# Kernel tuning notes

Measured on AMD Instinct MI355X. Metric: run time of the kernel, lower is better.

Reference implementation:

```python
import jax, jax.numpy as jnp
import numpy as np

B, S, E, D, H = 4, 2048, 512, 64, 8
NEG = float(np.finfo(np.float64).min)  # tf uses tf.float64.min; overflows to -inf in fp32, same softmax effect


def setup_inputs() -> dict:
    key = jax.random.key(0)
    ks = jax.random.split(key, 6)
    std = 0.05  # tf.random_normal_initializer default stddev
    x = jax.random.normal(ks[0], (B, S, E), dtype=jnp.float32)
    Wq = jax.random.normal(ks[1], (H, E, D), dtype=jnp.float32) * std
    Wk = jax.random.normal(ks[2], (H, E, D), dtype=jnp.float32) * std
    Wvd = jax.random.normal(ks[3], (H, E, D), dtype=jnp.float32) * std
    Wvu = jax.random.normal(ks[4], (H, D, E), dtype=jnp.float32) * std
    Wo = jax.random.normal(ks[5], (H, 1), dtype=jnp.float32) * std
    return {"x": x, "Wq": Wq, "Wk": Wk, "Wvd": Wvd, "Wvu": Wvu, "Wo": Wo}


def reference(x, Wq, Wk, Wvd, Wvu, Wo):
    # Per-head projections, vectorized over the head axis h
    Q = jnp.einsum("bse,hed->bhsd", x, Wq)  # [B,H,S,D]
    K = jnp.einsum("bse,hed->bhsd", x, Wk)
    score = jnp.einsum("bhsd,bhtd->bhst", Q, K) / jnp.sqrt(jnp.float32(D))
    # tf.linalg.band_part(score, -1, 0): keep lower triangle (causal)
    tril = jnp.tril(jnp.ones((S, S), dtype=bool))
    score = jnp.where(tril, score, 0.0)
    # tf.where(score != 0, score, float64.min): masks zeros (incl. any exact-zero kept entries)
    score = jnp.where(score != 0, score, jnp.float32(NEG))
    attn = jax.nn.softmax(score, axis=-1)  # [B,H,S,S]
    # low-rank value projection: x @ (Wvdown @ Wvup) per head
    Wv = jnp.einsum("hed,hdf->hef", Wvd, Wvu)  # [H,E,E]
    V = jnp.einsum("bse,hef->bhsf", x, Wv)      # [B,H,S,E]
    heads = jnp.einsum("bhst,bhte->bhse", attn, V)  # [B,H,S,E]
    # stack on last axis then matmul with Wo[H,1] == weighted sum over heads
    out = jnp.einsum("bhse,h->bse", heads, Wo[:, 0])
    return out
```

## Files before the change

kernel.cpp:

```cpp
#include <hip/hip_runtime.h>
#include <math.h>
#include <type_traits>

namespace {
constexpr int B = 4, S = 2048, E = 512, D = 64, H = 8;
constexpr int KD = 512;

typedef short bf8 __attribute__((ext_vector_type(8)));
typedef short bf4 __attribute__((ext_vector_type(4)));
typedef float f4 __attribute__((ext_vector_type(4)));

__device__ __forceinline__ short f2bf(float f) {
  union { float f; unsigned u; } v; v.f = f;
  const unsigned r = v.u + 0x7fffu + ((v.u >> 16) & 1u);
  return (short)(r >> 16);
}

__device__ __forceinline__ unsigned cvt_pk_bf16(float a, float b) {
  unsigned r;
  asm("v_cvt_pk_bf16_f32 %0, %1, %2" : "=v"(r) : "v"(a), "v"(b));
  return r;
}

__device__ __forceinline__ void gload16(const void* g, void* l) {
  __builtin_amdgcn_global_load_lds(
      (const __attribute__((address_space(1))) unsigned int*)g,
      (__attribute__((address_space(3))) unsigned int*)l, 16, 0, 0);
}

__global__ __launch_bounds__(256) void prep_kernel(
    const float* __restrict__ x, const float* __restrict__ Wq,
    const float* __restrict__ Wk, const float* __restrict__ Wvd,
    const float* __restrict__ Wvu, const float* __restrict__ Wo,
    short* __restrict__ xb, short* __restrict__ WcatT,
    short* __restrict__ W2T) {
  __shared__ float T[64][65];
  const int bid = blockIdx.x;
  const int tid = threadIdx.x;
  if (bid < 2048) {
    const size_t i = ((size_t)bid * 256 + tid) * 8;
    const float4 v0 = *(const float4*)(x + i);
    const float4 v1 = *(const float4*)(x + i + 4);
    bf8 o;
    o[0] = f2bf(v0.x); o[1] = f2bf(v0.y); o[2] = f2bf(v0.z); o[3] = f2bf(v0.w);
    o[4] = f2bf(v1.x); o[5] = f2bf(v1.y); o[6] = f2bf(v1.z); o[7] = f2bf(v1.w);
    *(bf8*)(xb + i) = o;
  } else if (bid < 2240) {
    const int r = bid - 2048;
    const int cb = r >> 3, e0 = (r & 7) * 64;
    const int w = cb >> 3, h = cb & 7;
    const float* Wsel = (w == 0) ? Wq : (w == 1) ? Wk : Wvd;
    const float* Wp = Wsel + (size_t)h * E * D;
#pragma unroll
    for (int i = 0; i < 4; ++i) {
      const int f = tid + i * 256;
      const int rr = f >> 4, c4 = f & 15;
      const float4 v = *(const float4*)(Wp + (size_t)(e0 + rr) * D + c4 * 4);
      T[rr][c4 * 4 + 0] = v.x; T[rr][c4 * 4 + 1] = v.y;
      T[rr][c4 * 4 + 2] = v.z; T[rr][c4 * 4 + 3] = v.w;
    }
    __syncthreads();
#pragma unroll
    for (int i = 0; i < 4; ++i) {
      const int f = tid + i * 256;
      const int dr = f >> 4, e4 = f & 15;
      bf4 o;
#pragma unroll
      for (int j = 0; j < 4; ++j) o[j] = f2bf(T[e4 * 4 + j][dr]);
      *(bf4*)(WcatT + (size_t)(cb * 64 + dr) * KD + e0 + e4 * 4) = o;
    }
  } else {
    const int r = bid - 2240;
    const int h = r >> 3, e0 = (r & 7) * 64;
    const float wo = Wo[h];
#pragma unroll
    for (int i = 0; i < 4; ++i) {
      const int f = tid + i * 256;
      const int rr = f >> 4, c4 = f & 15;
      const float4 v = *(const float4*)(Wvu + ((size_t)h * D + rr) * E + e0 + c4 * 4);
      T[rr][c4 * 4 + 0] = v.x * wo; T[rr][c4 * 4 + 1] = v.y * wo;
      T[rr][c4 * 4 + 2] = v.z * wo; T[rr][c4 * 4 + 3] = v.w * wo;
    }
    __syncthreads();
#pragma unroll
    for (int i = 0; i < 4; ++i) {
      const int f = tid + i * 256;
      const int er = f >> 4, d4 = f & 15;
      bf4 o;
#pragma unroll
      for (int j = 0; j < 4; ++j) o[j] = f2bf(T[d4 * 4 + j][er]);
      *(bf4*)(W2T + (size_t)(e0 + er) * KD + h * 64 + d4 * 4) = o;
    }
  }
}

template <int MODE>
__global__ __launch_bounds__(256) void gemm_kernel(
    const short* __restrict__ A, const short* __restrict__ Bt,
    short* __restrict__ Qb, short* __restrict__ Kb, short* __restrict__ Vtg,
    float* __restrict__ Of) {
  const int row0 = blockIdx.x * 128;
  const int ct = blockIdx.y;
  const int tid = threadIdx.x;
  const int w = tid >> 6, l = tid & 63;
  const int wm = w >> 1, wn = w & 1;
  const int lr = l & 15, hi = l >> 4;

  __shared__ short As[128 * 64];
  __shared__ short Bs[128 * 64];

  const short* Ag = A + (size_t)row0 * KD;
  const short* Bg = Bt + (size_t)ct * 128 * KD;

  f4 acc[4][4] = {};
  for (int k0 = 0; k0 < KD; k0 += 64) {
    __syncthreads();
#pragma unroll
    for (int i = 0; i < 4; ++i) {
      const int f = i * 256 + tid;
      const int r = f >> 3, g = f & 7;
      gload16(Ag + (size_t)r * KD + k0 + ((g ^ (r & 7)) << 3), &As[f * 8]);
    }
#pragma unroll
    for (int i = 0; i < 4; ++i) {
      const int f = i * 256 + tid;
      const int r = f >> 3, g = f & 7;
      gload16(Bg + (size_t)r * KD + k0 + ((g ^ (r & 7)) << 3), &Bs[f * 8]);
    }
    __syncthreads();

    bf8 af[4][2], bfv[4][2];
#pragma unroll
    for (int t = 0; t < 4; ++t) {
#pragma unroll
      for (int kh = 0; kh < 2; ++kh) {
        const int ar = wm * 64 + t * 16 + lr;
        af[t][kh] = *(const bf8*)&As[ar * 64 + (((kh * 4 + hi) ^ (ar & 7)) << 3)];
        const int br = wn * 64 + t * 16 + lr;
        bfv[t][kh] = *(const bf8*)&Bs[br * 64 + (((kh * 4 + hi) ^ (br & 7)) << 3)];
      }
    }
#pragma unroll
    for (int mt = 0; mt < 4; ++mt)
#pragma unroll
      for (int nt = 0; nt < 4; ++nt) {
        acc[mt][nt] =
            __builtin_amdgcn_mfma_f32_16x16x32_bf16(af[mt][0], bfv[nt][0], acc[mt][nt], 0, 0, 0);
        acc[mt][nt] =
            __builtin_amdgcn_mfma_f32_16x16x32_bf16(af[mt][1], bfv[nt][1], acc[mt][nt], 0, 0, 0);
      }
  }

  if constexpr (MODE == 0) {
#pragma unroll
    for (int nt = 0; nt < 4; ++nt) {
      const int gc = ct * 128 + wn * 64 + nt * 16 + lr;
      const int cb = gc >> 6, d = gc & 63;
      const int h = cb & 7;
      if (cb < 16) {
        short* Out = (cb < 8) ? Qb : Kb;
#pragma unroll
        for (int mt = 0; mt < 4; ++mt)
#pragma unroll
          for (int reg = 0; reg < 4; ++reg) {
            const int grow = row0 + wm * 64 + mt * 16 + hi * 4 + reg;
            const int b = grow >> 11, s = grow & (S - 1);
            Out[(((size_t)(b * H + h) * S + s) << 6) + d] = f2bf(acc[mt][nt][reg]);
          }
      } else {
        const int hswap = ((d >> 3) & 1) << 2;
#pragma unroll
        for (int mt = 0; mt < 4; ++mt) {
          const int grow0 = row0 + wm * 64 + mt * 16 + hi * 4;
          const int b = grow0 >> 11, s0 = (grow0 & (S - 1)) ^ hswap;
          bf4 o;
#pragma unroll
          for (int reg = 0; reg < 4; ++reg) o[reg] = f2bf(acc[mt][nt][reg]);
          *(bf4*)(Vtg + (((size_t)(b * H + h) * D + d) << 11) + s0) = o;
        }
      }
    }
  } else {
#pragma unroll
    for (int mt = 0; mt < 4; ++mt)
#pragma unroll
      for (int reg = 0; reg < 4; ++reg) {
        const int grow = row0 + wm * 64 + mt * 16 + hi * 4 + reg;
        float* orow = Of + (size_t)grow * 512 + ct * 128 + wn * 64;
#pragma unroll
        for (int nt = 0; nt < 4; ++nt) orow[nt * 16 + lr] = acc[mt][nt][reg];
      }
  }
}

__global__ __launch_bounds__(256) void attn_kernel(
    const short* __restrict__ Qb, const short* __restrict__ Kb,
    const short* __restrict__ Vt, short* __restrict__ PVb) {
  const int bh = blockIdx.x;
  const int j = blockIdx.y;
  const int qtA = j, qtB = 31 - j;
  const int nA = j + 1;
  const int b = bh >> 3, h = bh & 7;
  const int tid = threadIdx.x;
  const int w = tid >> 6, l = tid & 63;
  const int lr = l & 15, hi = l >> 4;

  __shared__ short Ks[4][64 * 64];
  __shared__ short Vs[4][64 * 64];

  const short* QgA = Qb + ((size_t)bh * S + qtA * 64 + w * 16 + lr) * D;
  const short* QgB = Qb + ((size_t)bh * S + qtB * 64 + w * 16 + lr) * D;
  const bf8 qA0 = *(const bf8*)(QgA + hi * 8);
  const bf8 qA1 = *(const bf8*)(QgA + 32 + hi * 8);
  const bf8 qB0 = *(const bf8*)(QgB + hi * 8);
  const bf8 qB1 = *(const bf8*)(QgB + 32 + hi * 8);

  const short* Kg = Kb + (size_t)bh * S * D;
  const short* Vg = Vt + (size_t)bh * D * S;

  const int sr = tid >> 3, sg = tid & 7;
  const int sswz = (sg ^ (sr & 7)) << 3;
  const int sr2 = sr + 32, sswz2 = (sg ^ (sr2 & 7)) << 3;
  const short* kg0 = Kg + (size_t)sr * D + sswz;
  const short* kg1 = Kg + (size_t)sr2 * D + sswz2;
  const short* vg0 = Vg + (size_t)sr * S + sswz;
  const short* vg1 = Vg + (size_t)sr2 * S + sswz2;

  const int e7 = lr & 7;
  const int kla0 = lr * 128 + ((hi ^ e7) << 4);
  const int kla1 = kla0 ^ 64;
  const int x7 = (hi >> 1) ^ e7;
  const int swaph = ((hi & 1) ^ ((lr >> 3) & 1)) << 3;
  int vla[4];
#pragma unroll
  for (int np = 0; np < 4; ++np)
    vla[np] = lr * 128 + (((2 * np) ^ x7) << 4) + swaph;

  float lsum4[4] = {};
  f4 accO[4] = {};

  auto step = [&](int buf, bf8 q0, bf8 q1, auto diag_c) {
    constexpr bool DIAG = decltype(diag_c)::value;
    const char* Klb = (const char*)Ks[buf];
    const char* Vlb = (const char*)Vs[buf];
    f4 accS[4] = {};
    __builtin_amdgcn_s_setprio(1);
#pragma unroll
    for (int n = 0; n < 4; ++n) {
      const bf8 k0 = *(const bf8*)(Klb + kla0 + n * 2048);
      const bf8 k1 = *(const bf8*)(Klb + kla1 + n * 2048);
      accS[n] = __builtin_amdgcn_mfma_f32_16x16x32_bf16(k0, q0, accS[n], 0, 0, 0);
      accS[n] = __builtin_amdgcn_mfma_f32_16x16x32_bf16(k1, q1, accS[n], 0, 0, 0);
    }
    __builtin_amdgcn_s_setprio(0);

    bf4 pa[4];
#pragma unroll
    for (int n = 0; n < 4; ++n) {
      float p[4];
#pragma unroll
      for (int reg = 0; reg < 4; ++reg) {
        float pv = __expf(fmaf(accS[n][reg], 0.125f, -12.0f));
        if constexpr (DIAG) {
          const bool ok = (n * 16 + hi * 4 + reg) <= (w * 16 + lr);
          pv = ok ? pv : 0.f;
        }
        p[reg] = pv;
        lsum4[reg] += pv;
      }
      union { int2 i; bf4 v; } u;
      u.i.x = (int)cvt_pk_bf16(p[0], p[1]);
      u.i.y = (int)cvt_pk_bf16(p[2], p[3]);
      pa[n] = u.v;
    }

    __builtin_amdgcn_s_setprio(1);
#pragma unroll
    for (int np = 0; np < 4; ++np) {
#pragma unroll
      for (int ne = 0; ne < 4; ++ne) {
        const bf4 vf = *(const bf4*)(Vlb + vla[np] + ne * 2048);
        accO[ne] = __builtin_amdgcn_mfma_f32_16x16x16bf16_1k(pa[np], vf, accO[ne], 0, 0, 0);
      }
    }
    __builtin_amdgcn_s_setprio(0);
  };

  auto epi = [&](int qt) {
    float lv = (lsum4[0] + lsum4[1]) + (lsum4[2] + lsum4[3]);
    lv += __shfl_xor(lv, 16);
    lv += __shfl_xor(lv, 32);
#pragma unroll
    for (int reg = 0; reg < 4; ++reg) {
      const float lq = __shfl(lv, hi * 4 + reg);
      const float inv = 1.f / lq;
      const int s = qt * 64 + w * 16 + hi * 4 + reg;
      short* op = PVb + (size_t)(b * S + s) * (H * D) + h * D;
#pragma unroll
      for (int n = 0; n < 4; ++n) op[n * 16 + lr] = f2bf(accO[n][reg] * inv);
    }
  };

  auto issue_chunk = [&](int c) {
    const int kt = (c < nA) ? c : c - nA;
    const size_t ko = (size_t)kt << 12;
    const size_t vo = (size_t)kt << 6;
    const int bb = c & 3;
    gload16(kg0 + ko, &Ks[bb][tid * 8]);
    gload16(kg1 + ko, &Ks[bb][(256 + tid) * 8]);
    gload16(vg0 + vo, &Vs[bb][tid * 8]);
    gload16(vg1 + vo, &Vs[bb][(256 + tid) * 8]);
  };

  auto do_chunk = [&](int c) {
    const int bb = c & 3;
    if (c < nA) {
      if (c == nA - 1) {
        step(bb, qA0, qA1, std::true_type{});
        epi(qtA);
#pragma unroll
        for (int n = 0; n < 4; ++n) accO[n] = f4{0.f, 0.f, 0.f, 0.f};
        lsum4[0] = lsum4[1] = lsum4[2] = lsum4[3] = 0.f;
      } else {
        step(bb, qA0, qA1, std::false_type{});
      }
    } else {
      if (c == 32) step(bb, qB0, qB1, std::true_type{});
      else         step(bb, qB0, qB1, std::false_type{});
    }
  };

  issue_chunk(0);
  issue_chunk(1);

  for (int s = 0; s < 17; ++s) {
    if (s > 0) {
      __builtin_amdgcn_s_barrier();
      __builtin_amdgcn_sched_barrier(0);
    }
    const int c0 = 2 * s, c1 = c0 + 1;
    const int p0 = c0 + 2, p1 = c0 + 3;
    if (p0 < 33) issue_chunk(p0);
    if (p1 < 33) issue_chunk(p1);
    if (p1 < 33) {
      asm volatile("s_waitcnt vmcnt(8)" ::: "memory");
    } else if (p0 < 33) {
      asm volatile("s_waitcnt vmcnt(4)" ::: "memory");
    } else {
      asm volatile("s_waitcnt vmcnt(0)" ::: "memory");
    }
    __builtin_amdgcn_sched_barrier(0);
    __builtin_amdgcn_s_barrier();
    __builtin_amdgcn_sched_barrier(0);

    do_chunk(c0);
    if (c1 < 33) do_chunk(c1);
  }
  epi(qtB);
}

}

extern "C" void kernel_launch(void* const* d_in, const int* in_sizes, int n_in,
                              void* d_out, int out_size, void* d_ws, size_t ws_size,
                              hipStream_t stream) {
  const float* x   = (const float*)d_in[0];
  const float* Wq  = (const float*)d_in[1];
  const float* Wk  = (const float*)d_in[2];
  const float* Wvd = (const float*)d_in[3];
  const float* Wvu = (const float*)d_in[4];
  const float* Wo  = (const float*)d_in[5];
  float* out = (float*)d_out;

  const size_t nqk = (size_t)B * H * S * D;
  short* xb    = (short*)d_ws;
  short* Qb    = xb + nqk;
  short* Kb    = Qb + nqk;
  short* Vtg   = Kb + nqk;
  short* PVb   = Vtg + nqk;
  short* WcatT = PVb + nqk;
  short* W2T   = WcatT + 1536 * KD;

  prep_kernel<<<dim3(2304), 256, 0, stream>>>(x, Wq, Wk, Wvd, Wvu, Wo,
                                              xb, WcatT, W2T);
  gemm_kernel<0><<<dim3(64, 12), 256, 0, stream>>>(xb, WcatT, Qb, Kb, Vtg, nullptr);
  attn_kernel<<<dim3(B * H, 16), 256, 0, stream>>>(Qb, Kb, Vtg, PVb);
  gemm_kernel<1><<<dim3(64, 4), 256, 0, stream>>>(PVb, W2T, nullptr, nullptr, nullptr, out);
}
```

Measured before the change: 82.98 us.

## Split KV chunks across two wave groups per attention block, merge via LDS

The attention kernel now runs 512 threads per block. Two groups of four waves each process alternate 64-row KV tiles from a shared 128-row double-buffered stage, and their partial output accumulators and row sums are merged through LDS at the end. This adds more waves per block to hide MFMA and load latency and halves the serial chunk chain per wave, at the cost of an extra LDS reduction and higher register and LDS pressure. The 1/sqrt(D) scale is also folded into the bf16 Wq weights in the prep kernel. That removes the per-element fma and the -12 offset before exp, which slightly raises overflow headroom risk.

```diff
diff --git a/kernel.cpp b/kernel.cpp
--- a/kernel.cpp
+++ b/kernel.cpp
@@ -51,6 +51,7 @@
     const int w = cb >> 3, h = cb & 7;
     const float* Wsel = (w == 0) ? Wq : (w == 1) ? Wk : Wvd;
     const float* Wp = Wsel + (size_t)h * E * D;
+    const float qs = (cb < 8) ? 0.125f : 1.0f;
 #pragma unroll
     for (int i = 0; i < 4; ++i) {
       const int f = tid + i * 256;
@@ -66,7 +67,7 @@
       const int dr = f >> 4, e4 = f & 15;
       bf4 o;
 #pragma unroll
-      for (int j = 0; j < 4; ++j) o[j] = f2bf(T[e4 * 4 + j][dr]);
+      for (int j = 0; j < 4; ++j) o[j] = f2bf(T[e4 * 4 + j][dr] * qs);
       *(bf4*)(WcatT + (size_t)(cb * 64 + dr) * KD + e0 + e4 * 4) = o;
     }
   } else {
@@ -193,23 +194,25 @@
   }
 }
 
-__global__ __launch_bounds__(256) void attn_kernel(
+__global__ __launch_bounds__(512, 4) void attn_kernel(
     const short* __restrict__ Qb, const short* __restrict__ Kb,
     const short* __restrict__ Vt, short* __restrict__ PVb) {
   const int bh = blockIdx.x;
   const int j = blockIdx.y;
   const int qtA = j, qtB = 31 - j;
-  const int nA = j + 1;
+  const int nA = j + 1, nB = 32 - j;
+  const int sA = (nA + 1) >> 1;
   const int b = bh >> 3, h = bh & 7;
   const int tid = threadIdx.x;
   const int w = tid >> 6, l = tid & 63;
+  const int wl = w & 3, g2 = w >> 2;
   const int lr = l & 15, hi = l >> 4;
 
-  __shared__ short Ks[4][64 * 64];
-  __shared__ short Vs[4][64 * 64];
-
-  const short* QgA = Qb + ((size_t)bh * S + qtA * 64 + w * 16 + lr) * D;
-  const short* QgB = Qb + ((size_t)bh * S + qtB * 64 + w * 16 + lr) * D;
+  __shared__ short Ks[2][128 * 64];
+  __shared__ short Vs[2][128 * 64];
+
+  const short* QgA = Qb + ((size_t)bh * S + qtA * 64 + wl * 16 + lr) * D;
+  const short* QgB = Qb + ((size_t)bh * S + qtB * 64 + wl * 16 + lr) * D;
   const bf8 qA0 = *(const bf8*)(QgA + hi * 8);
   const bf8 qA1 = *(const bf8*)(QgA + 32 + hi * 8);
   const bf8 qB0 = *(const bf8*)(QgB + hi * 8);
@@ -220,11 +223,9 @@
 
   const int sr = tid >> 3, sg = tid & 7;
   const int sswz = (sg ^ (sr & 7)) << 3;
-  const int sr2 = sr + 32, sswz2 = (sg ^ (sr2 & 7)) << 3;
   const short* kg0 = Kg + (size_t)sr * D + sswz;
-  const short* kg1 = Kg + (size_t)sr2 * D + sswz2;
+  const short* kg1 = Kg + (size_t)(sr + 64) * D + sswz;
   const short* vg0 = Vg + (size_t)sr * S + sswz;
-  const short* vg1 = Vg + (size_t)sr2 * S + sswz2;
 
   const int e7 = lr & 7;
   const int kla0 = lr * 128 + ((hi ^ e7) << 4);
@@ -235,14 +236,25 @@
 #pragma unroll
   for (int np = 0; np < 4; ++np)
     vla[np] = lr * 128 + (((2 * np) ^ x7) << 4) + swaph;
-
-  float lsum4[4] = {};
-  f4 accO[4] = {};
-
-  auto step = [&](int buf, bf8 q0, bf8 q1, auto diag_c) {
+  const int gofs = g2 * 8192;
+
+  float lsA[4] = {}, lsB[4] = {};
+  f4 accA[4] = {}, accB[4] = {};
+
+  auto stage = [&](int snext, int bb) {
+    const int kt0 = (snext < sA) ? 2 * snext : 2 * (snext - sA);
+    const size_t ko = (size_t)kt0 << 12;
+    const size_t vo = (size_t)kt0 << 6;
+    gload16(kg0 + ko, &Ks[bb][tid * 8]);
+    gload16(kg1 + ko, &Ks[bb][(512 + tid) * 8]);
+    gload16(vg0 + vo, &Vs[bb][tid * 8]);
+    gload16(vg0 + vo + 64, &Vs[bb][(512 + tid) * 8]);
+  };
+
+  auto step = [&](int bb, bf8 q0, bf8 q1, f4* aO, float* ls, auto diag_c) {
     constexpr bool DIAG = decltype(diag_c)::value;
-    const char* Klb = (const char*)Ks[buf];
-    const char* Vlb = (const char*)Vs[buf];
+    const char* Klb = (const char*)Ks[bb] + gofs;
+    const char* Vlb = (const char*)Vs[bb] + gofs;
     f4 accS[4] = {};
     __builtin_amdgcn_s_setprio(1);
 #pragma unroll
@@ -260,13 +272,13 @@
       float p[4];
 #pragma unroll
       for (int reg = 0; reg < 4; ++reg) {
-        float pv = __expf(fmaf(accS[n][reg], 0.125f, -12.0f));
+        float pv = __expf(accS[n][reg]);
         if constexpr (DIAG) {
-          const bool ok = (n * 16 + hi * 4 + reg) <= (w * 16 + lr);
+          const bool ok = (n * 16 + hi * 4 + reg) <= (wl * 16 + lr);
           pv = ok ? pv : 0.f;
         }
         p[reg] = pv;
-        lsum4[reg] += pv;
+        ls[reg] += pv;
       }
       union { int2 i; bf4 v; } u;
       u.i.x = (int)cvt_pk_bf16(p[0], p[1]);
@@ -280,71 +292,36 @@
 #pragma unroll
       for (int ne = 0; ne < 4; ++ne) {
         const bf4 vf = *(const bf4*)(Vlb + vla[np] + ne * 2048);
-        accO[ne] = __builtin_amdgcn_mfma_f32_16x16x16bf16_1k(pa[np], vf, accO[ne], 0, 0, 0);
+        aO[ne] = __builtin_amdgcn_mfma_f32_16x16x16bf16_1k(pa[np], vf, aO[ne], 0, 0, 0);
       }
     }
     __builtin_amdgcn_s_setprio(0);
   };
 
-  auto epi = [&](int qt) {
-    float lv = (lsum4[0] + lsum4[1]) + (lsum4[2] + lsum4[3]);
+  auto epi = [&](int qt, f4* aO, float* ls) {
+    float lv = (ls[0] + ls[1]) + (ls[2] + ls[3]);
     lv += __shfl_xor(lv, 16);
     lv += __shfl_xor(lv, 32);
 #pragma unroll
     for (int reg = 0; reg < 4; ++reg) {
       const float lq = __shfl(lv, hi * 4 + reg);
       const float inv = 1.f / lq;
-      const int s = qt * 64 + w * 16 + hi * 4 + reg;
+      const int s = qt * 64 + wl * 16 + hi * 4 + reg;
       short* op = PVb + (size_t)(b * S + s) * (H * D) + h * D;
 #pragma unroll
-      for (int n = 0; n < 4; ++n) op[n * 16 + lr] = f2bf(accO[n][reg] * inv);
+      for (int n = 0; n < 4; ++n) op[n * 16 + lr] = f2bf(aO[n][reg] * inv);
     }
   };
 
-  auto issue_chunk = [&](int c) {
-    const int kt = (c < nA) ? c : c - nA;
-    const size_t ko = (size_t)kt << 12;
-    const size_t vo = (size_t)kt << 6;
-    const int bb = c & 3;
-    gload16(kg0 + ko, &Ks[bb][tid * 8]);
-    gload16(kg1 + ko, &Ks[bb][(256 + tid) * 8]);
-    gload16(vg0 + vo, &Vs[bb][tid * 8]);
-    gload16(vg1 + vo, &Vs[bb][(256 + tid) * 8]);
-  };
-
-  auto do_chunk = [&](int c) {
-    const int bb = c & 3;
-    if (c < nA) {
-      if (c == nA - 1) {
-        step(bb, qA0, qA1, std::true_type{});
-        epi(qtA);
-#pragma unroll
-        for (int n = 0; n < 4; ++n) accO[n] = f4{0.f, 0.f, 0.f, 0.f};
-        lsum4[0] = lsum4[1] = lsum4[2] = lsum4[3] = 0.f;
-      } else {
-        step(bb, qA0, qA1, std::false_type{});
-      }
-    } else {
-      if (c == 32) step(bb, qB0, qB1, std::true_type{});
-      else         step(bb, qB0, qB1, std::false_type{});
-    }
-  };
-
-  issue_chunk(0);
-  issue_chunk(1);
+  stage(0, 0);
 
   for (int s = 0; s < 17; ++s) {
     if (s > 0) {
       __builtin_amdgcn_s_barrier();
       __builtin_amdgcn_sched_barrier(0);
     }
-    const int c0 = 2 * s, c1 = c0 + 1;
-    const int p0 = c0 + 2, p1 = c0 + 3;
-    if (p0 < 33) issue_chunk(p0);
-    if (p1 < 33) issue_chunk(p1);
-    if (p1 < 33) {
-      asm volatile("s_waitcnt vmcnt(8)" ::: "memory");
-    } else if (p0 < 33) {
+    if (s < 16) {
+      stage(s + 1, (s + 1) & 1);
       asm volatile("s_waitcnt vmcnt(4)" ::: "memory");
     } else {
       asm volatile("s_waitcnt vmcnt(0)" ::: "memory");
@@ -353,10 +330,59 @@
     __builtin_amdgcn_s_barrier();
     __builtin_amdgcn_sched_barrier(0);
 
-    do_chunk(c0);
-    if (c1 < 33) do_chunk(c1);
-  }
-  epi(qtB);
+    const int bb = s & 1;
+    if (s < sA) {
+      const int c = 2 * s + g2;
+      if (c < nA) {
+        if (c == nA - 1) step(bb, qA0, qA1, accA, lsA, std::true_type{});
+        else             step(bb, qA0, qA1, accA, lsA, std::false_type{});
+      }
+    } else {
+      const int c = 2 * (s - sA) + g2;
+      if (c < nB) {
+        if (c == nB - 1) step(bb, qB0, qB1, accB, lsB, std::true_type{});
+        else             step(bb, qB0, qB1, accB, lsB, std::false_type{});
+      }
+    }
+  }
+
+  __syncthreads();
+  float* cbA = (float*)&Ks[0][0];
+  float* cbB = (float*)&Vs[0][0];
+  const int slot = (wl * 64 + l) * 20;
+  if (g2 == 1) {
+#pragma unroll
+    for (int n = 0; n < 4; ++n)
+#pragma unroll
+      for (int reg = 0; reg < 4; ++reg) cbA[slot + n * 4 + reg] = accA[n][reg];
+#pragma unroll
+    for (int reg = 0; reg < 4; ++reg) cbA[slot + 16 + reg] = lsA[reg];
+  } else {
+#pragma unroll
+    for (int n = 0; n < 4; ++n)
+#pragma unroll
+      for (int reg = 0; reg < 4; ++reg) cbB[slot + n * 4 + reg] = accB[n][reg];
+#pragma unroll
+    for (int reg = 0; reg < 4; ++reg) cbB[slot + 16 + reg] = lsB[reg];
+  }
+  __syncthreads();
+  if (g2 == 0) {
+#pragma unroll
+    for (int n = 0; n < 4; ++n)
+#pragma unroll
+      for (int reg = 0; reg < 4; ++reg) accA[n][reg] += cbA[slot + n * 4 + reg];
+#pragma unroll
+    for (int reg = 0; reg < 4; ++reg) lsA[reg] += cbA[slot + 16 + reg];
+    epi(qtA, accA, lsA);
+  } else {
+#pragma unroll
+    for (int n = 0; n < 4; ++n)
+#pragma unroll
+      for (int reg = 0; reg < 4; ++reg) accB[n][reg] += cbB[slot + n * 4 + reg];
+#pragma unroll
+    for (int reg = 0; reg < 4; ++reg) lsB[reg] += cbB[slot + 16 + reg];
+    epi(qtB, accB, lsB);
+  }
 }
 
 }
@@ -384,6 +410,6 @@
   prep_kernel<<<dim3(2304), 256, 0, stream>>>(x, Wq, Wk, Wvd, Wvu, Wo,
                                               xb, WcatT, W2T);
   gemm_kernel<0><<<dim3(64, 12), 256, 0, stream>>>(xb, WcatT, Qb, Kb, Vtg, nullptr);
-  attn_kernel<<<dim3(B * H, 16), 256, 0, stream>>>(Qb, Kb, Vtg, PVb);
+  attn_kernel<<<dim3(B * H, 16), 512, 0, stream>>>(Qb, Kb, Vtg, PVb);
   gemm_kernel<1><<<dim3(64, 4), 256, 0, stream>>>(PVb, W2T, nullptr, nullptr, nullptr, out);
 }
```

Result: faster. 75.30 us, median of 2 (-9.3%).
